# Kernel optimization log

Hardware: AMD Instinct MI355X
Metric: run time of the kernel (lower is better)

Reference implementation:

```python
import jax, jax.numpy as jnp
import numpy as np

B, T, D, U = 32, 1024, 2048, 1024

def setup_inputs() -> dict:
    key = jax.random.key(0)
    ks = jax.random.split(key, 8)
    s_d = 1.0 / np.sqrt(D)
    s_u = 1.0 / np.sqrt(U)
    return {
        "query": jax.random.normal(ks[0], (B, D), dtype=jnp.float32),
        "values": jax.random.normal(ks[1], (B, T, D), dtype=jnp.float32),
        "W1": jax.random.normal(ks[2], (D, U), dtype=jnp.float32) * s_d,
        "b1": jnp.zeros((U,), dtype=jnp.float32),
        "W2": jax.random.normal(ks[3], (D, U), dtype=jnp.float32) * s_d,
        "b2": jnp.zeros((U,), dtype=jnp.float32),
        "V": jax.random.normal(ks[4], (U, 1), dtype=jnp.float32) * s_u,
        "bv": jnp.zeros((1,), dtype=jnp.float32),
    }

def reference(query, values, W1, b1, W2, b2, V, bv):
    # keys: (B, T, U); query proj broadcast over time axis
    keys_proj = jnp.einsum('btd,du->btu', values, W1) + b1
    query_proj = (query @ W2 + b2)[:, None, :]          # (B, 1, U)
    score = jnp.tanh(keys_proj + query_proj) @ V + bv   # (B, T, 1)
    attention_weights = jax.nn.softmax(score, axis=1)   # (B, T, 1)
    context_vector = jnp.sum(attention_weights * values, axis=1)  # (B, D)
    return (context_vector, attention_weights)
```

## Files before the change

kernel.cpp:

```cpp
#include <hip/hip_runtime.h>
#include <math.h>

#define BB 32
#define TS 1024
#define DD 2048
#define UU 1024

typedef _Float16 f16x8 __attribute__((ext_vector_type(8)));
typedef _Float16 f16x2 __attribute__((ext_vector_type(2)));
typedef __fp16 fp16x2 __attribute__((ext_vector_type(2)));
typedef float f32x4 __attribute__((ext_vector_type(4)));

union H8 { f16x8 v; f16x2 p[4]; };

static __device__ inline f16x2 pk(float a, float b) {
  fp16x2 r = __builtin_amdgcn_cvt_pkrtz(a, b);
  return __builtin_bit_cast(f16x2, r);
}

static __device__ inline void gld16(const _Float16* g, _Float16* l) {
  __builtin_amdgcn_global_load_lds(
      (const __attribute__((address_space(1))) void*)g,
      (__attribute__((address_space(3))) void*)l, 16, 0, 0);
}

__global__ void zero_kernel(float* __restrict__ p) {
  p[blockIdx.x * 1024 + threadIdx.x] = 0.f;
}

__global__ __launch_bounds__(512) void qproj_kernel(
    const float* __restrict__ query, const float* __restrict__ W2,
    const float* __restrict__ b1, const float* __restrict__ b2,
    float* __restrict__ qpb) {
  __shared__ float part[3][128];
  const int b = blockIdx.x >> 3, u0 = (blockIdx.x & 7) * 128;
  const int tid = threadIdx.x, ul = tid & 127, sl = tid >> 7;
  const float* q = query + b * DD + sl * 512;
  const float* w = W2 + (size_t)(sl * 512) * UU + u0 + ul;
  float acc = 0.f;
#pragma unroll 8
  for (int d = 0; d < 512; ++d) acc += q[d] * w[(size_t)d * UU];
  if (sl) part[sl - 1][ul] = acc;
  __syncthreads();
  if (sl == 0) {
    int u = u0 + ul;
    qpb[b * UU + u] = acc + part[0][ul] + part[1][ul] + part[2][ul] + b1[u] + b2[u];
  }
}

__global__ __launch_bounds__(256) void pack_values_kernel(
    const float* __restrict__ v, _Float16* __restrict__ vhp) {
  __shared__ _Float16 img[8192];
  const int mTile = blockIdx.x >> 5;
  const int kc = blockIdx.x & 31;
  const int tid = threadIdx.x;

#pragma unroll
  for (int i = 0; i < 4; ++i) {
    int idx = i * 256 + tid;
    int row = idx >> 3, khi = idx & 7;
    const float* src = v + ((size_t)(mTile * 128 + row)) * DD + kc * 64 + khi * 8;
    float4 x = *(const float4*)src;
    float4 y = *(const float4*)(src + 4);
    H8 h;
    h.p[0] = pk(x.x, x.y); h.p[1] = pk(x.z, x.w);
    h.p[2] = pk(y.x, y.y); h.p[3] = pk(y.z, y.w);
    *(f16x8*)&img[(khi * 128 + (row ^ khi)) * 8] = h.v;
  }
  __syncthreads();

  _Float16* out = vhp + ((size_t)mTile * 32 + kc) * 8192;
#pragma unroll
  for (int i = 0; i < 4; ++i) {
    int p = i * 256 + tid;
    int khi = p >> 7, row = p & 127;
    *(f16x8*)(out + (size_t)p * 8) = *(const f16x8*)&img[(khi * 128 + (row ^ khi)) * 8];
  }
}

__global__ __launch_bounds__(256) void pack_w1_kernel(
    const float* __restrict__ W1, _Float16* __restrict__ w1p) {
  __shared__ _Float16 img[8192];
  const int nTile = blockIdx.x >> 5;
  const int kc = blockIdx.x & 31;
  const int tid = threadIdx.x;

#pragma unroll
  for (int i = 0; i < 32; ++i) {
    int idx = i * 256 + tid;
    int ul = idx & 127, kl = idx >> 7;
    float x = W1[(size_t)(kc * 64 + kl) * UU + nTile * 128 + ul];
    int khi = kl >> 3, klo = kl & 7;
    img[(khi * 128 + (ul ^ khi)) * 8 + klo] = (_Float16)x;
  }
  __syncthreads();

  _Float16* out = w1p + ((size_t)nTile * 32 + kc) * 8192;
#pragma unroll
  for (int i = 0; i < 4; ++i) {
    int p = i * 256 + tid;
    int khi = p >> 7, row = p & 127;
    *(f16x8*)(out + (size_t)p * 8) = *(const f16x8*)&img[(khi * 128 + (row ^ khi)) * 8];
  }
}

__global__ __launch_bounds__(256) void score_gemm_p_kernel(
    const _Float16* __restrict__ vhp, const _Float16* __restrict__ w1p,
    const float* __restrict__ qpb, const float* __restrict__ V,
    float* __restrict__ score) {
  __shared__ _Float16 aS[8192];
  __shared__ _Float16 bS[8192];

  const int tid = threadIdx.x;
  const int r = blockIdx.x & 7, q = blockIdx.x >> 3;
  const int mTile = r * 32 + (q >> 3);
  const int nTile = q & 7;
  const int mBase = mTile * 128, nBase = nTile * 128;

  const int lane = tid & 63, wave = tid >> 6;
  const int wm = (wave & 1) * 64, wn = (wave >> 1) * 64;
  const int quad = lane >> 4, c16 = lane & 15;

  const _Float16* gA = vhp + (size_t)mTile * 32 * 8192 + lane * 8;
  const _Float16* gB = w1p + (size_t)nTile * 32 * 8192 + lane * 8;

  f32x4 acc[4][4];
#pragma unroll
  for (int mi = 0; mi < 4; ++mi)
#pragma unroll
    for (int ni = 0; ni < 4; ++ni) acc[mi][ni] = (f32x4)0.f;

  for (int kc = 0; kc < 32; ++kc) {
    __syncthreads();
#pragma unroll
    for (int j = 0; j < 4; ++j) {
      int s = wave * 4 + j;
      gld16(gA + (size_t)kc * 8192 + s * 512, &aS[s * 512]);
      gld16(gB + (size_t)kc * 8192 + s * 512, &bS[s * 512]);
    }
    __syncthreads();

#pragma unroll
    for (int h = 0; h < 2; ++h) {
      f16x8 af[4], bf[4];
#pragma unroll
      for (int i = 0; i < 4; ++i) {
        af[i] = *(const f16x8*)&aS[((h * 4 + quad) * 128 + wm + i * 16 + c16) * 8];
        bf[i] = *(const f16x8*)&bS[((h * 4 + quad) * 128 + wn + i * 16 + c16) * 8];
      }
#pragma unroll
      for (int mi = 0; mi < 4; ++mi)
#pragma unroll
        for (int ni = 0; ni < 4; ++ni)
          acc[mi][ni] = __builtin_amdgcn_mfma_f32_16x16x32_f16(
              af[mi], bf[ni], acc[mi][ni], 0, 0, 0);
    }
  }

  const int b = mBase >> 10;
  float qv[4], vv[4];
#pragma unroll
  for (int ni = 0; ni < 4; ++ni) {
    int ug = nBase + wn + ni * 16 + c16;
    qv[ni] = qpb[b * UU + ug];
    vv[ni] = V[ug];
  }
#pragma unroll
  for (int mi = 0; mi < 4; ++mi) {
#pragma unroll
    for (int reg = 0; reg < 4; ++reg) {
      float p = tanhf(acc[mi][0][reg] + qv[0]) * vv[0] +
                tanhf(acc[mi][1][reg] + qv[1]) * vv[1] +
                tanhf(acc[mi][2][reg] + qv[2]) * vv[2] +
                tanhf(acc[mi][3][reg] + qv[3]) * vv[3];
      p += __shfl_xor(p, 1, 64);
      p += __shfl_xor(p, 2, 64);
      p += __shfl_xor(p, 4, 64);
      p += __shfl_xor(p, 8, 64);
      if (c16 == 0) {
        int mrow = mBase + wm + mi * 16 + quad * 4 + reg;
        atomicAdd(&score[mrow], p);
      }
    }
  }
}

__global__ __launch_bounds__(256) void score_gemm_kernel(
    const float* __restrict__ values, const float* __restrict__ W1,
    const float* __restrict__ qpb, const float* __restrict__ V,
    float* __restrict__ score) {
  __shared__ _Float16 aS[4 * 128 * 8];
  __shared__ _Float16 bS[4 * 128 * 8];

  const int tid = threadIdx.x;
  const int mBase = (blockIdx.x >> 3) * 128;
  const int nBase = (blockIdx.x & 7) * 128;

  const int am = tid >> 1;
  const int akh = (tid & 1) * 16;
  const float* aG = values + (size_t)(mBase + am) * DD + akh;
  const int aOff0 = (((tid & 1) * 2) * 128 + am) * 8;
  const int bu2 = (tid & 63) * 2;
  const int bkq = tid >> 6;
  const float* bG = W1 + (size_t)(bkq * 8) * UU + nBase + bu2;
  const int bOff0 = (bkq * 128 + bu2) * 8;

  const int lane = tid & 63;
  const int wave = tid >> 6;
  const int wm = (wave & 1) * 64;
  const int wn = (wave >> 1) * 64;
  const int quad = lane >> 4;
  const int c16 = lane & 15;

  f32x4 acc[4][4];
#pragma unroll
  for (int mi = 0; mi < 4; ++mi)
#pragma unroll
    for (int ni = 0; ni < 4; ++ni) acc[mi][ni] = (f32x4)0.f;

  for (int k0 = 0; k0 < DD; k0 += 32) {
    float4 a0 = *(const float4*)(aG + k0 + 0);
    float4 a1 = *(const float4*)(aG + k0 + 4);
    float4 a2 = *(const float4*)(aG + k0 + 8);
    float4 a3 = *(const float4*)(aG + k0 + 12);
    const float* bRow = bG + (size_t)k0 * UU;
    float2 g0 = *(const float2*)(bRow + 0 * UU);
    float2 g1 = *(const float2*)(bRow + 1 * UU);
    float2 g2 = *(const float2*)(bRow + 2 * UU);
    float2 g3 = *(const float2*)(bRow + 3 * UU);
    float2 g4 = *(const float2*)(bRow + 4 * UU);
    float2 g5 = *(const float2*)(bRow + 5 * UU);
    float2 g6 = *(const float2*)(bRow + 6 * UU);
    float2 g7 = *(const float2*)(bRow + 7 * UU);

    __syncthreads();

    H8 ha0, ha1, hb0, hb1;
    ha0.p[0] = pk(a0.x, a0.y); ha0.p[1] = pk(a0.z, a0.w);
    ha0.p[2] = pk(a1.x, a1.y); ha0.p[3] = pk(a1.z, a1.w);
    ha1.p[0] = pk(a2.x, a2.y); ha1.p[1] = pk(a2.z, a2.w);
    ha1.p[2] = pk(a3.x, a3.y); ha1.p[3] = pk(a3.z, a3.w);
    *(f16x8*)&aS[aOff0] = ha0.v;
    *(f16x8*)&aS[aOff0 + 1024] = ha1.v;

    hb0.p[0] = pk(g0.x, g1.x); hb0.p[1] = pk(g2.x, g3.x);
    hb0.p[2] = pk(g4.x, g5.x); hb0.p[3] = pk(g6.x, g7.x);
    hb1.p[0] = pk(g0.y, g1.y); hb1.p[1] = pk(g2.y, g3.y);
    hb1.p[2] = pk(g4.y, g5.y); hb1.p[3] = pk(g6.y, g7.y);
    *(f16x8*)&bS[bOff0] = hb0.v;
    *(f16x8*)&bS[bOff0 + 8] = hb1.v;

    __syncthreads();

    f16x8 af[4], bf[4];
#pragma unroll
    for (int i = 0; i < 4; ++i) {
      af[i] = *(const f16x8*)&aS[(quad * 128 + wm + i * 16 + c16) * 8];
      bf[i] = *(const f16x8*)&bS[(quad * 128 + wn + i * 16 + c16) * 8];
    }
#pragma unroll
    for (int mi = 0; mi < 4; ++mi)
#pragma unroll
      for (int ni = 0; ni < 4; ++ni)
        acc[mi][ni] = __builtin_amdgcn_mfma_f32_16x16x32_f16(
            af[mi], bf[ni], acc[mi][ni], 0, 0, 0);
  }

  const int b = mBase >> 10;
  float qv[4], vv[4];
#pragma unroll
  for (int ni = 0; ni < 4; ++ni) {
    int ug = nBase + wn + ni * 16 + c16;
    qv[ni] = qpb[b * UU + ug];
    vv[ni] = V[ug];
  }
#pragma unroll
  for (int mi = 0; mi < 4; ++mi) {
#pragma unroll
    for (int reg = 0; reg < 4; ++reg) {
      float p = tanhf(acc[mi][0][reg] + qv[0]) * vv[0] +
                tanhf(acc[mi][1][reg] + qv[1]) * vv[1] +
                tanhf(acc[mi][2][reg] + qv[2]) * vv[2] +
                tanhf(acc[mi][3][reg] + qv[3]) * vv[3];
      p += __shfl_xor(p, 1, 64);
      p += __shfl_xor(p, 2, 64);
      p += __shfl_xor(p, 4, 64);
      p += __shfl_xor(p, 8, 64);
      if (c16 == 0) {
        int mrow = mBase + wm + mi * 16 + quad * 4 + reg;
        atomicAdd(&score[mrow], p);
      }
    }
  }
}

__global__ __launch_bounds__(256) void softmax_kernel(float* __restrict__ sw) {
  __shared__ float red[256];
  const int b = blockIdx.x;
  const int tid = threadIdx.x;
  float* s = sw + b * TS;

  float vals[4];
  float m = -1e30f;
#pragma unroll
  for (int i = 0; i < 4; ++i) {
    vals[i] = s[tid + 256 * i];
    m = fmaxf(m, vals[i]);
  }
  red[tid] = m;
  __syncthreads();
  for (int off = 128; off > 0; off >>= 1) {
    if (tid < off) red[tid] = fmaxf(red[tid], red[tid + off]);
    __syncthreads();
  }
  m = red[0];
  __syncthreads();

  float sum = 0.f;
#pragma unroll
  for (int i = 0; i < 4; ++i) {
    vals[i] = expf(vals[i] - m);
    sum += vals[i];
  }
  red[tid] = sum;
  __syncthreads();
  for (int off = 128; off > 0; off >>= 1) {
    if (tid < off) red[tid] += red[tid + off];
    __syncthreads();
  }
  const float inv = 1.f / red[0];
#pragma unroll
  for (int i = 0; i < 4; ++i) s[tid + 256 * i] = vals[i] * inv;
}

__global__ __launch_bounds__(1024) void context_kernel(
    const float* __restrict__ values, const float* __restrict__ weights,
    float* __restrict__ context) {
  __shared__ float wl[TS];
  __shared__ float part[7][128];
  const int b = blockIdx.x >> 4;
  const int d0 = (blockIdx.x & 15) * 128;
  const int tid = threadIdx.x;
  const int slice = tid >> 7;
  const int dl = tid & 127;

  wl[tid] = weights[b * TS + tid];
  __syncthreads();

  const float* vb = values + ((size_t)b * TS + slice * 128) * DD + d0 + dl;
  float acc = 0.f;
#pragma unroll 8
  for (int t = 0; t < 128; ++t) acc += wl[slice * 128 + t] * vb[(size_t)t * DD];

  if (slice) part[slice - 1][dl] = acc;
  __syncthreads();
  if (slice == 0) {
    float s = acc;
#pragma unroll
    for (int i = 0; i < 7; ++i) s += part[i][dl];
    context[b * DD + d0 + dl] = s;
  }
}

extern "C" void kernel_launch(void* const* d_in, const int* in_sizes, int n_in,
                              void* d_out, int out_size, void* d_ws, size_t ws_size,
                              hipStream_t stream) {
  const float* query  = (const float*)d_in[0];
  const float* values = (const float*)d_in[1];
  const float* W1     = (const float*)d_in[2];
  const float* b1     = (const float*)d_in[3];
  const float* W2     = (const float*)d_in[4];
  const float* b2     = (const float*)d_in[5];
  const float* V      = (const float*)d_in[6];

  float* out = (float*)d_out;
  float* context = out;
  float* weights = out + BB * DD;

  float* qpb   = context;
  float* score = weights;

  const size_t need = (size_t)BB * TS * DD * 2 + (size_t)DD * UU * 2;
  const bool big_ws = ws_size >= need;

  zero_kernel<<<TS * BB / 1024, 1024, 0, stream>>>(score);
  qproj_kernel<<<BB * 8, 512, 0, stream>>>(query, W2, b1, b2, qpb);

  if (big_ws) {
    _Float16* vhp = (_Float16*)d_ws;
    _Float16* w1p = vhp + (size_t)BB * TS * DD;
    pack_values_kernel<<<256 * 32, 256, 0, stream>>>(values, vhp);
    pack_w1_kernel<<<8 * 32, 256, 0, stream>>>(W1, w1p);
    score_gemm_p_kernel<<<(BB * TS / 128) * (UU / 128), 256, 0, stream>>>(
        vhp, w1p, qpb, V, score);
  } else {
    score_gemm_kernel<<<(BB * TS / 128) * (UU / 128), 256, 0, stream>>>(
        values, W1, qpb, V, score);
  }

  softmax_kernel<<<BB, 256, 0, stream>>>(score);
  context_kernel<<<BB * 16, 1024, 0, stream>>>(values, weights, context);
}
```

Before: 665.2 us.

## Use fast exp2-based tanh, rework query projection and vectorize context kernel

Three separate changes. The tanh in the score GEMM epilogue becomes an exp2/rcp approximation to cut transcendental cost. The query projection now splits D across 64 blocks, each covering all 32 batches with W2 loaded once, and accumulates into a zeroed qpb buffer with atomics. The context kernel uses float4 loads over 256-wide D tiles with 16 time slices. Together these aim to cut ALU and memory-load cost, but the fast tanh is less accurate and the atomic accumulation makes results depend on ordering.

```diff
diff --git a/kernel.cpp b/kernel.cpp
--- a/kernel.cpp
+++ b/kernel.cpp
@@ -18,6 +18,11 @@
   return __builtin_bit_cast(f16x2, r);
 }
 
+static __device__ inline float fast_tanh(float x) {
+  float e = __builtin_amdgcn_exp2f(x * 2.885390081777927f);
+  return 1.f - 2.f * __builtin_amdgcn_rcpf(1.f + e);
+}
+
 static __device__ inline void gld16(const _Float16* g, _Float16* l) {
   __builtin_amdgcn_global_load_lds(
       (const __attribute__((address_space(1))) void*)g,
@@ -28,24 +33,44 @@
   p[blockIdx.x * 1024 + threadIdx.x] = 0.f;
 }
 
-__global__ __launch_bounds__(512) void qproj_kernel(
+__global__ __launch_bounds__(256) void qproj_kernel(
     const float* __restrict__ query, const float* __restrict__ W2,
     const float* __restrict__ b1, const float* __restrict__ b2,
     float* __restrict__ qpb) {
-  __shared__ float part[3][128];
-  const int b = blockIdx.x >> 3, u0 = (blockIdx.x & 7) * 128;
-  const int tid = threadIdx.x, ul = tid & 127, sl = tid >> 7;
-  const float* q = query + b * DD + sl * 512;
-  const float* w = W2 + (size_t)(sl * 512) * UU + u0 + ul;
-  float acc = 0.f;
-#pragma unroll 8
-  for (int d = 0; d < 512; ++d) acc += q[d] * w[(size_t)d * UU];
-  if (sl) part[sl - 1][ul] = acc;
-  __syncthreads();
-  if (sl == 0) {
-    int u = u0 + ul;
-    qpb[b * UU + u] = acc + part[0][ul] + part[1][ul] + part[2][ul] + b1[u] + b2[u];
-  }
+  __shared__ float qs[32][256];
+  const int u0 = (blockIdx.x & 7) * 128;
+  const int dsl = blockIdx.x >> 3;
+  const int d0 = dsl * 256;
+  const int tid = threadIdx.x;
+  const int ul = tid & 127, half = tid >> 7;
+
+  for (int i = tid; i < 32 * 64; i += 256) {
+    int b = i >> 6, dq = i & 63;
+    *(float4*)&qs[b][dq * 4] = *(const float4*)(query + b * DD + d0 + dq * 4);
+  }
+  __syncthreads();
+
+  float acc[32];
+#pragma unroll
+  for (int b = 0; b < 32; ++b) acc[b] = 0.f;
+
+  const float* wcol = W2 + (size_t)(d0 + half * 128) * UU + u0 + ul;
+  for (int dd = 0; dd < 128; dd += 4) {
+    float w0 = wcol[(size_t)(dd + 0) * UU];
+    float w1 = wcol[(size_t)(dd + 1) * UU];
+    float w2 = wcol[(size_t)(dd + 2) * UU];
+    float w3 = wcol[(size_t)(dd + 3) * UU];
+#pragma unroll
+    for (int b = 0; b < 32; ++b) {
+      float4 q4 = *(const float4*)&qs[b][half * 128 + dd];
+      acc[b] += q4.x * w0 + q4.y * w1 + q4.z * w2 + q4.w * w3;
+    }
+  }
+
+  const int u = u0 + ul;
+  const float bias = (dsl == 0 && half == 0) ? (b1[u] + b2[u]) : 0.f;
+#pragma unroll
+  for (int b = 0; b < 32; ++b) atomicAdd(&qpb[b * UU + u], acc[b] + bias);
 }
 
 __global__ __launch_bounds__(256) void pack_values_kernel(
@@ -169,10 +194,10 @@
   for (int mi = 0; mi < 4; ++mi) {
 #pragma unroll
     for (int reg = 0; reg < 4; ++reg) {
-      float p = tanhf(acc[mi][0][reg] + qv[0]) * vv[0] +
-                tanhf(acc[mi][1][reg] + qv[1]) * vv[1] +
-                tanhf(acc[mi][2][reg] + qv[2]) * vv[2] +
-                tanhf(acc[mi][3][reg] + qv[3]) * vv[3];
+      float p = fast_tanh(acc[mi][0][reg] + qv[0]) * vv[0] +
+                fast_tanh(acc[mi][1][reg] + qv[1]) * vv[1] +
+                fast_tanh(acc[mi][2][reg] + qv[2]) * vv[2] +
+                fast_tanh(acc[mi][3][reg] + qv[3]) * vv[3];
       p += __shfl_xor(p, 1, 64);
       p += __shfl_xor(p, 2, 64);
       p += __shfl_xor(p, 4, 64);
@@ -278,10 +303,10 @@
   for (int mi = 0; mi < 4; ++mi) {
 #pragma unroll
     for (int reg = 0; reg < 4; ++reg) {
-      float p = tanhf(acc[mi][0][reg] + qv[0]) * vv[0] +
-                tanhf(acc[mi][1][reg] + qv[1]) * vv[1] +
-                tanhf(acc[mi][2][reg] + qv[2]) * vv[2] +
-                tanhf(acc[mi][3][reg] + qv[3]) * vv[3];
+      float p = fast_tanh(acc[mi][0][reg] + qv[0]) * vv[0] +
+                fast_tanh(acc[mi][1][reg] + qv[1]) * vv[1] +
+                fast_tanh(acc[mi][2][reg] + qv[2]) * vv[2] +
+                fast_tanh(acc[mi][3][reg] + qv[3]) * vv[3];
       p += __shfl_xor(p, 1, 64);
       p += __shfl_xor(p, 2, 64);
       p += __shfl_xor(p, 4, 64);
@@ -337,28 +362,34 @@
     const float* __restrict__ values, const float* __restrict__ weights,
     float* __restrict__ context) {
   __shared__ float wl[TS];
-  __shared__ float part[7][128];
-  const int b = blockIdx.x >> 4;
-  const int d0 = (blockIdx.x & 15) * 128;
-  const int tid = threadIdx.x;
-  const int slice = tid >> 7;
-  const int dl = tid & 127;
+  __shared__ float4 part[15][64];
+  const int b = blockIdx.x >> 3;
+  const int d0 = (blockIdx.x & 7) * 256;
+  const int tid = threadIdx.x;
+  const int slice = tid >> 6, dl = tid & 63;
 
   wl[tid] = weights[b * TS + tid];
   __syncthreads();
 
-  const float* vb = values + ((size_t)b * TS + slice * 128) * DD + d0 + dl;
-  float acc = 0.f;
+  const float* vb = values + ((size_t)b * TS + slice * 64) * DD + d0 + dl * 4;
+  float4 acc = {0.f, 0.f, 0.f, 0.f};
 #pragma unroll 8
-  for (int t = 0; t < 128; ++t) acc += wl[slice * 128 + t] * vb[(size_t)t * DD];
+  for (int t = 0; t < 64; ++t) {
+    float w = wl[slice * 64 + t];
+    float4 v4 = *(const float4*)(vb + (size_t)t * DD);
+    acc.x += w * v4.x; acc.y += w * v4.y;
+    acc.z += w * v4.z; acc.w += w * v4.w;
+  }
 
   if (slice) part[slice - 1][dl] = acc;
   __syncthreads();
   if (slice == 0) {
-    float s = acc;
-#pragma unroll
-    for (int i = 0; i < 7; ++i) s += part[i][dl];
-    context[b * DD + d0 + dl] = s;
+#pragma unroll
+    for (int i = 0; i < 15; ++i) {
+      float4 p = part[i][dl];
+      acc.x += p.x; acc.y += p.y; acc.z += p.z; acc.w += p.w;
+    }
+    *(float4*)(context + b * DD + d0 + dl * 4) = acc;
   }
 }
 
@@ -383,8 +414,8 @@
   const size_t need = (size_t)BB * TS * DD * 2 + (size_t)DD * UU * 2;
   const bool big_ws = ws_size >= need;
 
-  zero_kernel<<<TS * BB / 1024, 1024, 0, stream>>>(score);
-  qproj_kernel<<<BB * 8, 512, 0, stream>>>(query, W2, b1, b2, qpb);
+  zero_kernel<<<96, 1024, 0, stream>>>(out);
+  qproj_kernel<<<64, 256, 0, stream>>>(query, W2, b1, b2, qpb);
 
   if (big_ws) {
     _Float16* vhp = (_Float16*)d_ws;
@@ -399,5 +430,5 @@
   }
 
   softmax_kernel<<<BB, 256, 0, stream>>>(score);
-  context_kernel<<<BB * 16, 1024, 0, stream>>>(values, weights, context);
-}
+  context_kernel<<<BB * 8, 1024, 0, stream>>>(values, weights, context);
+}
```

New measurement: 649.7 us. 1.02x faster.
